# Optimization experiments

Hardware: AMD Instinct MI355X
Metric: run time of the kernel (lower is better)

Reference implementation:

```python
import jax, jax.numpy as jnp
import numpy as np

NUM_BINS = 8
TAIL = 3.0
MBW = 0.001  # min_bin_width
MBH = 0.001  # min_bin_height
MD = 0.001   # min_derivative


def _conv(x, w, b):
    y = jax.lax.conv_general_dilated(x, w, (1, 1), 'SAME',
                                     dimension_numbers=('NCHW', 'OIHW', 'NCHW'))
    return y + b[None, :, None, None]


def _convnet(x, w1, b1, w2, b2, w3, b3):
    h = jax.nn.relu(_conv(x, w1, b1))
    h = jax.nn.relu(_conv(h, w2, b2))
    return _conv(h, w3, b3)


def _rqs_forward(x, uw, uh, ud):
    # x: (N,), uw/uh: (N, num_bins), ud: (N, num_bins-1)
    nb = uw.shape[-1]
    inside = (x >= -TAIL) & (x <= TAIL)
    xin = jnp.clip(x, -TAIL, TAIL)
    # linear tails: pad derivatives so boundary slope == 1
    const = float(np.log(np.exp(1.0 - MD) - 1.0))
    ud = jnp.pad(ud, ((0, 0), (1, 1)), constant_values=const)

    widths = jax.nn.softmax(uw, axis=-1)
    widths = MBW + (1.0 - MBW * nb) * widths
    cumw = jnp.pad(jnp.cumsum(widths, axis=-1), ((0, 0), (1, 0)))
    cumw = 2.0 * TAIL * cumw - TAIL
    cumw = cumw.at[:, 0].set(-TAIL).at[:, -1].set(TAIL)
    widths = cumw[:, 1:] - cumw[:, :-1]

    heights = jax.nn.softmax(uh, axis=-1)
    heights = MBH + (1.0 - MBH * nb) * heights
    cumh = jnp.pad(jnp.cumsum(heights, axis=-1), ((0, 0), (1, 0)))
    cumh = 2.0 * TAIL * cumh - TAIL
    cumh = cumh.at[:, 0].set(-TAIL).at[:, -1].set(TAIL)
    heights = cumh[:, 1:] - cumh[:, :-1]

    deriv = MD + jax.nn.softplus(ud)  # (N, nb+1)

    # searchsorted: locate bin of each element
    idx = jnp.clip(jnp.sum((xin[:, None] >= cumw).astype(jnp.int32), axis=-1) - 1, 0, nb - 1)
    gather = lambda t: jnp.take_along_axis(t, idx[:, None], axis=-1)[:, 0]

    in_cw = gather(cumw)
    in_w = gather(widths)
    in_ch = gather(cumh)
    in_h = gather(heights)
    in_delta = gather(heights / widths)
    d0 = gather(deriv)
    d1 = gather(deriv[:, 1:])

    theta = (xin - in_cw) / in_w
    tom = theta * (1.0 - theta)
    numer = in_h * (in_delta * theta ** 2 + d0 * tom)
    denom = in_delta + (d0 + d1 - 2.0 * in_delta) * tom
    y = in_ch + numer / denom
    dnum = in_delta ** 2 * (d1 * theta ** 2 + 2.0 * in_delta * tom + d0 * (1.0 - theta) ** 2)
    lad = jnp.log(dnum) - 2.0 * jnp.log(denom)

    y = jnp.where(inside, y, x)
    lad = jnp.where(inside, lad, 0.0)
    return y, lad


def setup_inputs() -> dict:
    key = jax.random.key(0)
    ks = jax.random.split(key, 9)
    B, C, H, W = 32, 12, 64, 64
    hidden = 128
    cond_c = C // 3
    out_spline = C * (3 * NUM_BINS - 1)
    x = jax.random.normal(ks[0], (B, C, H, W), dtype=jnp.float32)
    logdet = jnp.zeros((B,), dtype=jnp.float32)
    conditioning = jax.random.normal(ks[1], (B, cond_c, H, W), dtype=jnp.float32)
    w1 = jax.random.normal(ks[2], (hidden, C + cond_c, 3, 3), dtype=jnp.float32) * 0.05
    b1 = jnp.zeros((hidden,), dtype=jnp.float32)
    w2 = jax.random.normal(ks[3], (hidden, hidden, 1, 1), dtype=jnp.float32) * 0.05
    b2 = jnp.zeros((hidden,), dtype=jnp.float32)
    w3 = jax.random.normal(ks[4], (out_spline, hidden, 3, 3), dtype=jnp.float32) * 0.01
    b3 = jnp.zeros((out_spline,), dtype=jnp.float32)
    return {"x": x, "logdet": logdet, "conditioning": conditioning,
            "w1": w1, "b1": b1, "w2": w2, "b2": b2, "w3": w3, "b3": b3}


def reference(x, logdet, conditioning, w1, b1, w2, b2, w3, b3):
    B, C, H, W = x.shape
    net_in = jnp.concatenate([x, conditioning], axis=1)
    params = _convnet(net_in, w1, b1, w2, b2, w3, b3)  # (B, C*(3nb-1), H, W)
    params = params.reshape(B, C, 3 * NUM_BINS - 1, H, W)
    params = params.transpose(0, 1, 3, 4, 2).reshape(B * C * H * W, 3 * NUM_BINS - 1)
    uw = params[:, :NUM_BINS]
    uh = params[:, NUM_BINS:2 * NUM_BINS]
    ud = params[:, 2 * NUM_BINS:]
    y_flat, lad_flat = _rqs_forward(x.reshape(-1), uw, uh, ud)
    y = y_flat.reshape(B, C, H, W)
    logdet_out = logdet + lad_flat.reshape(B, -1).sum(axis=1)
    return y, logdet_out
```

## Files before the change

### kernel.cpp

```cpp
#include <hip/hip_runtime.h>
#include <math.h>


#define NPIX 4096
#define NY   1572864

typedef _Float16 half8 __attribute__((ext_vector_type(8)));
typedef _Float16 half4 __attribute__((ext_vector_type(4)));
typedef float f32x4 __attribute__((ext_vector_type(4)));

#define ASYNC16(gsrc, ldst) \
  __builtin_amdgcn_global_load_lds((const __attribute__((address_space(1))) unsigned int*)(gsrc), \
                                   (__attribute__((address_space(3))) unsigned int*)(ldst), 16, 0, 0)

#define H2P_PLANE 4356
#define H2P_IDX(b, cc, pp) ((((size_t)(b) * 4 + (cc)) * H2P_PLANE + (pp)) << 5)
#define XH_IDX(b, pp) (((size_t)(b) * H2P_PLANE + (pp)) << 5)

__global__ __launch_bounds__(256) void prep_k(
    const float* __restrict__ w1, const float* __restrict__ w2,
    const float* __restrict__ w3, _Float16* __restrict__ w1h,
    _Float16* __restrict__ w2h, _Float16* __restrict__ w3h,
    const float* __restrict__ logdet, float* __restrict__ ld_out)
{
    const int i = blockIdx.x * 256 + threadIdx.x;
    if (i < 36864) {
        int k = i & 31, oc = (i >> 5) & 127, t = i >> 12;
        w1h[i] = (_Float16)((k < 16) ? w1[(oc * 16 + k) * 9 + t] : 0.f);
    }
    if (i < 16384) {
        int km = i & 31, oc = (i >> 5) & 127, ks = i >> 12;
        w2h[i] = (_Float16)w2[oc * 128 + ks * 32 + km];
    }
    {
        int cim = i & 31;
        int oc = (i >> 5) % 288;
        int tc = i / (288 * 32);
        int t = tc >> 2, cc = tc & 3;
        int c = oc / 24, j = oc % 24;
        int ci = cc * 32 + cim;
        float v = (j < 23) ? w3[((c * 23 + j) * 128 + ci) * 9 + t] : 0.f;
        w3h[i] = (_Float16)v;
    }
    if (i < 32) ld_out[i] = logdet[i];
}

__global__ __launch_bounds__(256) void xh_k(
    const float* __restrict__ x, const float* __restrict__ cond,
    _Float16* __restrict__ xh)
{
    const int i = blockIdx.x * 256 + threadIdx.x;
    if (i >= 139392) return;
    const int b = i / H2P_PLANE, pp = i % H2P_PLANE;
    const int pr = pp / 66, pc = pp % 66;
    const bool interior = (pr >= 1) && (pr <= 64) && (pc >= 1) && (pc <= 64);
    _Float16 v[32];
#pragma unroll
    for (int ci = 0; ci < 32; ++ci) v[ci] = (_Float16)0.f;
    if (interior) {
        const int p = (pr - 1) * 64 + (pc - 1);
#pragma unroll
        for (int ci = 0; ci < 12; ++ci)
            v[ci] = (_Float16)x[((size_t)(b * 12 + ci) << 12) + p];
#pragma unroll
        for (int ci = 0; ci < 4; ++ci)
            v[12 + ci] = (_Float16)cond[((size_t)(b * 4 + ci) << 12) + p];
    }
    _Float16* dst = xh + ((size_t)i << 5);
#pragma unroll
    for (int q = 0; q < 4; ++q) *(f32x4*)(dst + q * 8) = *(f32x4*)(v + q * 8);
}

__global__ __launch_bounds__(256) void zring_k(_Float16* __restrict__ h2p)
{
    const int i = blockIdx.x * 256 + threadIdx.x;
    if (i >= 133120) return;
    const int q = i & 3;
    const int rest = i >> 2;
    const int r = rest % 260;
    const int cc = (rest / 260) & 3;
    const int b = rest / 1040;
    int pp;
    if (r < 66)       pp = r;
    else if (r < 132) pp = 65 * 66 + (r - 66);
    else if (r < 196) pp = (r - 131) * 66;
    else              pp = (r - 195) * 66 + 65;
    f32x4 z = {0.f, 0.f, 0.f, 0.f};
    *(f32x4*)(h2p + H2P_IDX(b, cc, pp) + q * 8) = z;
}

__global__ __launch_bounds__(256, 2) void conv1_k(
    const _Float16* __restrict__ xh, const _Float16* __restrict__ w1h,
    const float* __restrict__ b1, _Float16* __restrict__ h1p)
{
    __shared__ __align__(16) char smem[73728];
    const int tid = threadIdx.x;
    const int wv = tid >> 6, lane = tid & 63;
    const int row16 = lane & 15, quad = lane >> 4;
    const int ptile = blockIdx.x;
    const int b = ptile >> 4;
    const int pim0 = (ptile & 15) << 8;
    const int h0 = pim0 >> 6;

#pragma unroll
    for (int k = 0; k < 18; ++k)
        ASYNC16(w1h + (size_t)(k * 256 + tid) * 8, smem + (k * 256 + wv * 64) * 16);

    f32x4 acc[4][8];
#pragma unroll
    for (int pt = 0; pt < 4; ++pt)
#pragma unroll
        for (int ot = 0; ot < 8; ++ot) acc[pt][ot] = (f32x4){0.f, 0.f, 0.f, 0.f};

    __syncthreads();
    const _Float16* wl = (const _Float16*)smem;

    for (int t = 0; t < 9; ++t) {
        const int dy = t / 3, dx = t % 3;
        const int pbase = (h0 + wv + dy) * 66 + dx + row16;
        half8 bf[4], af[8];
#pragma unroll
        for (int pt = 0; pt < 4; ++pt)
            bf[pt] = *(const half8*)(xh + XH_IDX(b, pbase + pt * 16) + quad * 8);
#pragma unroll
        for (int ot = 0; ot < 8; ++ot)
            af[ot] = *(const half8*)(wl + ((t * 128 + ot * 16 + row16) << 5) + quad * 8);
#pragma unroll
        for (int ot = 0; ot < 8; ++ot)
#pragma unroll
            for (int pt = 0; pt < 4; ++pt)
                acc[pt][ot] = __builtin_amdgcn_mfma_f32_16x16x32_f16(af[ot], bf[pt], acc[pt][ot], 0, 0, 0);
    }

    f32x4 bias[8];
#pragma unroll
    for (int ot = 0; ot < 8; ++ot) bias[ot] = *(const f32x4*)(b1 + ot * 16 + quad * 4);
#pragma unroll
    for (int pt = 0; pt < 4; ++pt) {
        const size_t pbase = ((size_t)((b << 12) + pim0 + wv * 64 + pt * 16 + row16)) << 7;
#pragma unroll
        for (int ot = 0; ot < 8; ++ot) {
            half4 v;
#pragma unroll
            for (int r = 0; r < 4; ++r)
                v[r] = (_Float16)fmaxf(acc[pt][ot][r] + bias[ot][r], 0.f);
            *(half4*)(h1p + pbase + ot * 16 + quad * 4) = v;
        }
    }
}

__global__ __launch_bounds__(256, 2) void conv2_k(
    const _Float16* __restrict__ h1p, const _Float16* __restrict__ w2h,
    const float* __restrict__ b2, _Float16* __restrict__ h2p)
{
    __shared__ __align__(16) char smem[33280];
    float* b2l = (float*)(smem + 32768);
    const int tid = threadIdx.x;
    const int wv = tid >> 6, lane = tid & 63;
    const int row16 = lane & 15, quad = lane >> 4;
    const int ptile = blockIdx.x;
    const int b = ptile >> 4;
    const int pim0 = (ptile & 15) << 8;

    if (tid < 128) b2l[tid] = b2[tid];
#pragma unroll
    for (int k = 0; k < 8; ++k) {
        const int c0 = k * 256 + wv * 64;
        ASYNC16(w2h + (size_t)(c0 + lane) * 8, smem + c0 * 16);
    }

    f32x4 acc[4][8];
#pragma unroll
    for (int pt = 0; pt < 4; ++pt)
#pragma unroll
        for (int ot = 0; ot < 8; ++ot) acc[pt][ot] = (f32x4){0.f, 0.f, 0.f, 0.f};

    const int pixbase = (b << 12) + pim0 + wv * 64;
    __syncthreads();

#pragma unroll
    for (int ks = 0; ks < 4; ++ks) {
        half8 bf[4], af[8];
#pragma unroll
        for (int pt = 0; pt < 4; ++pt)
            bf[pt] = *(const half8*)(h1p + ((size_t)(pixbase + pt * 16 + row16) << 7) + ks * 32 + quad * 8);
        const _Float16* wl = (const _Float16*)smem;
#pragma unroll
        for (int ot = 0; ot < 8; ++ot)
            af[ot] = *(const half8*)(wl + ((ks * 128 + ot * 16 + row16) << 5) + quad * 8);
#pragma unroll
        for (int ot = 0; ot < 8; ++ot)
#pragma unroll
            for (int pt = 0; pt < 4; ++pt)
                acc[pt][ot] = __builtin_amdgcn_mfma_f32_16x16x32_f16(af[ot], bf[pt], acc[pt][ot], 0, 0, 0);
    }

#pragma unroll
    for (int pt = 0; pt < 4; ++pt) {
        const int p = pim0 + wv * 64 + pt * 16 + row16;
        const int pp = ((p >> 6) + 1) * 66 + (p & 63) + 1;
#pragma unroll
        for (int ot = 0; ot < 8; ++ot) {
            const int oc0 = ot * 16 + quad * 4;
            half4 v;
#pragma unroll
            for (int r = 0; r < 4; ++r)
                v[r] = (_Float16)fmaxf(acc[pt][ot][r] + b2l[oc0 + r], 0.f);
            *(half4*)(h2p + H2P_IDX(b, oc0 >> 5, pp) + (oc0 & 31)) = v;
        }
    }
}

__device__ __forceinline__ void rqs_eval(const float* prm, float xv,
                                         float& yv_out, float& lad_out)
{
    const float xin = fminf(fmaxf(xv, -3.f), 3.f);

    float mw = prm[0], mh = prm[8];
#pragma unroll
    for (int j = 1; j < 8; ++j) { mw = fmaxf(mw, prm[j]); mh = fmaxf(mh, prm[8 + j]); }
    float ew[8], eh[8];
    float sw = 0.f, sh = 0.f;
#pragma unroll
    for (int j = 0; j < 8; ++j) {
        ew[j] = expf(prm[j] - mw);      sw += ew[j];
        eh[j] = expf(prm[8 + j] - mh);  sh += eh[j];
    }
    const float rw = 1.f / sw, rh = 1.f / sh;

    const float CONST_D = logf(expf(0.999f) - 1.f);

    float cumw = 0.f, cumh = 0.f;
    float cw_lo = -3.f, ch_lo = -3.f;
    float in_cw = 0.f, in_w = 1.f, in_ch = 0.f, in_h = 1.f, sd0 = 0.f, sd1 = 0.f;
#pragma unroll
    for (int i = 0; i < 8; ++i) {
        cumw += fmaf(0.992f, ew[i] * rw, 0.001f);
        cumh += fmaf(0.992f, eh[i] * rh, 0.001f);
        const float cw_hi = (i == 7) ? 3.f : fmaf(6.f, cumw, -3.f);
        const float ch_hi = (i == 7) ? 3.f : fmaf(6.f, cumh, -3.f);
        const bool sel = (xin >= cw_lo) && ((i == 7) || (xin < cw_hi));
        in_cw = sel ? cw_lo : in_cw;
        in_w  = sel ? (cw_hi - cw_lo) : in_w;
        in_ch = sel ? ch_lo : in_ch;
        in_h  = sel ? (ch_hi - ch_lo) : in_h;
        sd0   = sel ? ((i == 0) ? CONST_D : prm[16 + i - 1]) : sd0;
        sd1   = sel ? ((i == 7) ? CONST_D : prm[16 + i]) : sd1;
        cw_lo = cw_hi; ch_lo = ch_hi;
    }

    const float d0 = 0.001f + ((sd0 > 20.f) ? sd0 : log1pf(expf(sd0)));
    const float d1 = 0.001f + ((sd1 > 20.f) ? sd1 : log1pf(expf(sd1)));

    const float delta = in_h / in_w;
    const float theta = (xin - in_cw) / in_w;
    const float omt = 1.f - theta;
    const float tom = theta * omt;
    const float th2 = theta * theta;
    const float numer = in_h * (delta * th2 + d0 * tom);
    const float denom = delta + (d0 + d1 - 2.f * delta) * tom;
    float yv = in_ch + numer / denom;
    const float dnum = delta * delta * (d1 * th2 + 2.f * delta * tom + d0 * omt * omt);
    float lad = logf(dnum) - 2.f * logf(denom);

    const bool inside = (xv >= -3.f) && (xv <= 3.f);
    yv_out = inside ? yv : xv;
    lad_out = inside ? lad : 0.f;
}

__global__ __launch_bounds__(256, 2) void conv3_rqs_k(
    const _Float16* __restrict__ h2p, const _Float16* __restrict__ w3h,
    const float* __restrict__ b3, const float* __restrict__ x,
    float* __restrict__ y, float* __restrict__ ld_out)
{
    __shared__ __align__(16) char smem[44352];
    float* b3l = (float*)(smem + 43776);

    const int tid = threadIdx.x;
    const int wv = tid >> 6, lane = tid & 63;
    const int row16 = lane & 15, quad = lane >> 4;
    const int col = blockIdx.x;
    const int ptile = blockIdx.y;
    const int b = ptile >> 4;
    const int pim0 = (ptile & 15) << 8;
    const int h0 = pim0 >> 6;

    if (tid < 144) {
        const int c = tid / 24, j = tid % 24;
        b3l[tid] = (j < 23) ? b3[(col * 6 + c) * 23 + j] : 0.f;
    }

    f32x4 acc[4][9];
#pragma unroll
    for (int pt = 0; pt < 4; ++pt)
#pragma unroll
        for (int ot = 0; ot < 9; ++ot) acc[pt][ot] = (f32x4){0.f, 0.f, 0.f, 0.f};

    auto stage_wt = [&](int t, int cc, int buf) {
        const _Float16* g = w3h + ((size_t)((t * 4 + cc) * 288 + col * 144) << 5);
        char* wb = smem + 25344 + buf * 9216;
        ASYNC16(g + (size_t)tid * 8, wb + wv * 64 * 16);
        ASYNC16(g + (size_t)(256 + tid) * 8, wb + (256 + wv * 64) * 16);
        if (wv == 0) ASYNC16(g + (size_t)(512 + lane) * 8, wb + 512 * 16);
    };
    auto stage_act = [&](int cc) {
        const _Float16* ga = h2p + H2P_IDX(b, cc, h0 * 66);
#pragma unroll
        for (int k = 0; k < 6; ++k)
            ASYNC16(ga + (size_t)(k * 256 + tid) * 8, smem + (k * 256 + wv * 64) * 16);
        if (wv == 0 && lane < 48)
            ASYNC16(ga + (size_t)(1536 + lane) * 8, smem + 1536 * 16);
    };

    stage_act(0);
    stage_wt(0, 0, 0);

    for (int cc = 0; cc < 4; ++cc) {
        for (int t = 0; t < 9; ++t) {
            const int step = cc * 9 + t;
            __syncthreads();
            if (step + 1 < 36)
                stage_wt((t == 8) ? 0 : t + 1, (t == 8) ? cc + 1 : cc, (step + 1) & 1);
            const _Float16* act = (const _Float16*)smem;
            const _Float16* wt = (const _Float16*)(smem + 25344 + (step & 1) * 9216);
            const int dy = t / 3, dx = t % 3;
            const int lpp = (wv + dy) * 66 + dx + row16;
            half8 bf[4], af[9];
#pragma unroll
            for (int pt = 0; pt < 4; ++pt)
                bf[pt] = *(const half8*)(act + ((lpp + pt * 16) << 5) + quad * 8);
#pragma unroll
            for (int ot = 0; ot < 9; ++ot)
                af[ot] = *(const half8*)(wt + ((ot * 16 + row16) << 5) + quad * 8);
#pragma unroll
            for (int ot = 0; ot < 9; ++ot)
#pragma unroll
                for (int pt = 0; pt < 4; ++pt)
                    acc[pt][ot] = __builtin_amdgcn_mfma_f32_16x16x32_f16(af[ot], bf[pt], acc[pt][ot], 0, 0, 0);
            if (t == 8 && cc < 3) {
                __syncthreads();
                stage_act(cc + 1);
            }
        }
    }
    __syncthreads();

    float* epi = (float*)smem + wv * 2368;
    float lad_acc = 0.f;
#pragma unroll
    for (int pt = 0; pt < 4; ++pt) {
#pragma unroll
        for (int ot = 0; ot < 9; ++ot)
            *(f32x4*)(epi + row16 * 148 + ot * 16 + quad * 4) = acc[pt][ot];
        __syncthreads();
#pragma unroll 1
        for (int pass = 0; pass < 2; ++pass) {
            const int idx = pass * 64 + lane;
            if (idx < 96) {
                const int p16 = idx & 15, c = idx >> 4;
                float prm[23];
#pragma unroll
                for (int j = 0; j < 23; ++j)
                    prm[j] = epi[p16 * 148 + c * 24 + j] + b3l[c * 24 + j];
                const int tpix = wv * 64 + pt * 16 + p16;
                const size_t xi = (((size_t)(b * 12 + col * 6 + c)) << 12) + (pim0 + tpix);
                const float xv = x[xi];
                float yv, lad;
                rqs_eval(prm, xv, yv, lad);
                y[xi] = yv;
                lad_acc += lad;
            }
        }
        __syncthreads();
    }

#pragma unroll
    for (int off = 32; off > 0; off >>= 1) lad_acc += __shfl_down(lad_acc, off);
    if (lane == 0) atomicAdd(&ld_out[b], lad_acc);
}

extern "C" void kernel_launch(void* const* d_in, const int* in_sizes, int n_in,
                              void* d_out, int out_size, void* d_ws, size_t ws_size,
                              hipStream_t stream)
{
    const float* x      = (const float*)d_in[0];
    const float* logdet = (const float*)d_in[1];
    const float* cond   = (const float*)d_in[2];
    const float* w1     = (const float*)d_in[3];
    const float* b1     = (const float*)d_in[4];
    const float* w2     = (const float*)d_in[5];
    const float* b2     = (const float*)d_in[6];
    const float* w3     = (const float*)d_in[7];
    const float* b3     = (const float*)d_in[8];

    char* ws = (char*)d_ws;
    _Float16* h1p = (_Float16*)ws;
    _Float16* h2p = (_Float16*)(ws + 33554432);
    _Float16* xh  = (_Float16*)(ws + 33554432);
    _Float16* w1h = (_Float16*)(ws + 69238784);
    _Float16* w2h = (_Float16*)(ws + 69312512);
    _Float16* w3h = (_Float16*)(ws + 69345280);

    float* y      = (float*)d_out;
    float* ld_out = y + NY;

    prep_k<<<1296, 256, 0, stream>>>(w1, w2, w3, w1h, w2h, w3h, logdet, ld_out);
    xh_k<<<545, 256, 0, stream>>>(x, cond, xh);
    conv1_k<<<512, 256, 0, stream>>>(xh, w1h, b1, h1p);
    zring_k<<<520, 256, 0, stream>>>(h2p);
    conv2_k<<<512, 256, 0, stream>>>(h1p, w2h, b2, h2p);
    conv3_rqs_k<<<dim3(2, 512), 256, 0, stream>>>(h2p, w3h, b3, x, y, ld_out);
}
```

Baseline: 238.2 us.

## Fold small prep kernels into neighbors and speed up RQS epilogue

Merges the input-packing kernel into the weight prep kernel and moves h2p border zeroing into conv2, removing two launches. The RQS spline evaluation switches to fast intrinsics (__expf/__logf), a precomputed constant, a shared reciprocal, and vectorized LDS parameter loads. Block-wide barriers in the per-wave epilogue are replaced with a wave-local LDS wait, since each wave uses its own scratch region. Fast-math intrinsics slightly reduce accuracy.

Result: faster. 226.1 us (-5.1%).

```diff
diff --git a/kernel.cpp b/kernel.cpp
--- a/kernel.cpp
+++ b/kernel.cpp
@@ -17,11 +17,13 @@
 #define H2P_IDX(b, cc, pp) ((((size_t)(b) * 4 + (cc)) * H2P_PLANE + (pp)) << 5)
 #define XH_IDX(b, pp) (((size_t)(b) * H2P_PLANE + (pp)) << 5)
 
-__global__ __launch_bounds__(256) void prep_k(
+__global__ __launch_bounds__(256) void prep_xh_k(
     const float* __restrict__ w1, const float* __restrict__ w2,
     const float* __restrict__ w3, _Float16* __restrict__ w1h,
     _Float16* __restrict__ w2h, _Float16* __restrict__ w3h,
-    const float* __restrict__ logdet, float* __restrict__ ld_out)
+    const float* __restrict__ logdet, float* __restrict__ ld_out,
+    const float* __restrict__ x, const float* __restrict__ cond,
+    _Float16* __restrict__ xh)
 {
     const int i = blockIdx.x * 256 + threadIdx.x;
     if (i < 36864) {
@@ -43,50 +45,27 @@
         w3h[i] = (_Float16)v;
     }
     if (i < 32) ld_out[i] = logdet[i];
-}
-
-__global__ __launch_bounds__(256) void xh_k(
-    const float* __restrict__ x, const float* __restrict__ cond,
-    _Float16* __restrict__ xh)
-{
-    const int i = blockIdx.x * 256 + threadIdx.x;
-    if (i >= 139392) return;
-    const int b = i / H2P_PLANE, pp = i % H2P_PLANE;
-    const int pr = pp / 66, pc = pp % 66;
-    const bool interior = (pr >= 1) && (pr <= 64) && (pc >= 1) && (pc <= 64);
-    _Float16 v[32];
-#pragma unroll
-    for (int ci = 0; ci < 32; ++ci) v[ci] = (_Float16)0.f;
-    if (interior) {
-        const int p = (pr - 1) * 64 + (pc - 1);
-#pragma unroll
-        for (int ci = 0; ci < 12; ++ci)
-            v[ci] = (_Float16)x[((size_t)(b * 12 + ci) << 12) + p];
-#pragma unroll
-        for (int ci = 0; ci < 4; ++ci)
-            v[12 + ci] = (_Float16)cond[((size_t)(b * 4 + ci) << 12) + p];
-    }
-    _Float16* dst = xh + ((size_t)i << 5);
-#pragma unroll
-    for (int q = 0; q < 4; ++q) *(f32x4*)(dst + q * 8) = *(f32x4*)(v + q * 8);
-}
-
-__global__ __launch_bounds__(256) void zring_k(_Float16* __restrict__ h2p)
-{
-    const int i = blockIdx.x * 256 + threadIdx.x;
-    if (i >= 133120) return;
-    const int q = i & 3;
-    const int rest = i >> 2;
-    const int r = rest % 260;
-    const int cc = (rest / 260) & 3;
-    const int b = rest / 1040;
-    int pp;
-    if (r < 66)       pp = r;
-    else if (r < 132) pp = 65 * 66 + (r - 66);
-    else if (r < 196) pp = (r - 131) * 66;
-    else              pp = (r - 195) * 66 + 65;
-    f32x4 z = {0.f, 0.f, 0.f, 0.f};
-    *(f32x4*)(h2p + H2P_IDX(b, cc, pp) + q * 8) = z;
+
+    if (i < 139392) {
+        const int b = i / H2P_PLANE, pp = i % H2P_PLANE;
+        const int pr = pp / 66, pc = pp % 66;
+        const bool interior = (pr >= 1) && (pr <= 64) && (pc >= 1) && (pc <= 64);
+        _Float16 v[32];
+#pragma unroll
+        for (int ci = 0; ci < 32; ++ci) v[ci] = (_Float16)0.f;
+        if (interior) {
+            const int p = (pr - 1) * 64 + (pc - 1);
+#pragma unroll
+            for (int ci = 0; ci < 12; ++ci)
+                v[ci] = (_Float16)x[((size_t)(b * 12 + ci) << 12) + p];
+#pragma unroll
+            for (int ci = 0; ci < 4; ++ci)
+                v[12 + ci] = (_Float16)cond[((size_t)(b * 4 + ci) << 12) + p];
+        }
+        _Float16* dst = xh + ((size_t)i << 5);
+#pragma unroll
+        for (int q = 0; q < 4; ++q) *(f32x4*)(dst + q * 8) = *(f32x4*)(v + q * 8);
+    }
 }
 
 __global__ __launch_bounds__(256, 2) void conv1_k(
@@ -169,6 +148,28 @@
         ASYNC16(w2h + (size_t)(c0 + lane) * 8, smem + c0 * 16);
     }
 
+    {
+        const int base = blockIdx.x * 256 + tid;
+#pragma unroll
+        for (int rep = 0; rep < 2; ++rep) {
+            const int i = base + rep * 131072;
+            if (i < 133120) {
+                const int q = i & 3;
+                const int rest = i >> 2;
+                const int r = rest % 260;
+                const int cc2 = (rest / 260) & 3;
+                const int bb = rest / 1040;
+                int pp;
+                if (r < 66)       pp = r;
+                else if (r < 132) pp = 65 * 66 + (r - 66);
+                else if (r < 196) pp = (r - 131) * 66;
+                else              pp = (r - 195) * 66 + 65;
+                f32x4 z = {0.f, 0.f, 0.f, 0.f};
+                *(f32x4*)(h2p + H2P_IDX(bb, cc2, pp) + q * 8) = z;
+            }
+        }
+    }
+
     f32x4 acc[4][8];
 #pragma unroll
     for (int pt = 0; pt < 4; ++pt)
@@ -211,24 +212,25 @@
     }
 }
 
-__device__ __forceinline__ void rqs_eval(const float* prm, float xv,
+__device__ __forceinline__ void rqs_eval(const f32x4* pv, float xv,
                                          float& yv_out, float& lad_out)
 {
+#define PRM(j) (pv[(j) >> 2][(j) & 3])
     const float xin = fminf(fmaxf(xv, -3.f), 3.f);
 
-    float mw = prm[0], mh = prm[8];
-#pragma unroll
-    for (int j = 1; j < 8; ++j) { mw = fmaxf(mw, prm[j]); mh = fmaxf(mh, prm[8 + j]); }
+    float mw = PRM(0), mh = PRM(8);
+#pragma unroll
+    for (int j = 1; j < 8; ++j) { mw = fmaxf(mw, PRM(j)); mh = fmaxf(mh, PRM(8 + j)); }
     float ew[8], eh[8];
     float sw = 0.f, sh = 0.f;
 #pragma unroll
     for (int j = 0; j < 8; ++j) {
-        ew[j] = expf(prm[j] - mw);      sw += ew[j];
-        eh[j] = expf(prm[8 + j] - mh);  sh += eh[j];
+        ew[j] = __expf(PRM(j) - mw);      sw += ew[j];
+        eh[j] = __expf(PRM(8 + j) - mh);  sh += eh[j];
     }
     const float rw = 1.f / sw, rh = 1.f / sh;
 
-    const float CONST_D = logf(expf(0.999f) - 1.f);
+    const float CONST_D = 0.5397423f;
 
     float cumw = 0.f, cumh = 0.f;
     float cw_lo = -3.f, ch_lo = -3.f;
@@ -244,16 +246,17 @@
         in_w  = sel ? (cw_hi - cw_lo) : in_w;
         in_ch = sel ? ch_lo : in_ch;
         in_h  = sel ? (ch_hi - ch_lo) : in_h;
-        sd0   = sel ? ((i == 0) ? CONST_D : prm[16 + i - 1]) : sd0;
-        sd1   = sel ? ((i == 7) ? CONST_D : prm[16 + i]) : sd1;
+        sd0   = sel ? ((i == 0) ? CONST_D : PRM(16 + i - 1)) : sd0;
+        sd1   = sel ? ((i == 7) ? CONST_D : PRM(16 + i)) : sd1;
         cw_lo = cw_hi; ch_lo = ch_hi;
     }
 
-    const float d0 = 0.001f + ((sd0 > 20.f) ? sd0 : log1pf(expf(sd0)));
-    const float d1 = 0.001f + ((sd1 > 20.f) ? sd1 : log1pf(expf(sd1)));
-
-    const float delta = in_h / in_w;
-    const float theta = (xin - in_cw) / in_w;
+    const float d0 = 0.001f + ((sd0 > 20.f) ? sd0 : __logf(1.f + __expf(sd0)));
+    const float d1 = 0.001f + ((sd1 > 20.f) ? sd1 : __logf(1.f + __expf(sd1)));
+
+    const float r_inw = 1.f / in_w;
+    const float delta = in_h * r_inw;
+    const float theta = (xin - in_cw) * r_inw;
     const float omt = 1.f - theta;
     const float tom = theta * omt;
     const float th2 = theta * theta;
@@ -261,11 +264,12 @@
     const float denom = delta + (d0 + d1 - 2.f * delta) * tom;
     float yv = in_ch + numer / denom;
     const float dnum = delta * delta * (d1 * th2 + 2.f * delta * tom + d0 * omt * omt);
-    float lad = logf(dnum) - 2.f * logf(denom);
+    float lad = __logf(dnum) - 2.f * __logf(denom);
 
     const bool inside = (xv >= -3.f) && (xv <= 3.f);
     yv_out = inside ? yv : xv;
     lad_out = inside ? lad : 0.f;
+#undef PRM
 }
 
 __global__ __launch_bounds__(256, 2) void conv3_rqs_k(
@@ -352,26 +356,30 @@
 #pragma unroll
         for (int ot = 0; ot < 9; ++ot)
             *(f32x4*)(epi + row16 * 148 + ot * 16 + quad * 4) = acc[pt][ot];
-        __syncthreads();
+        asm volatile("s_waitcnt lgkmcnt(0)" ::: "memory");
+        __builtin_amdgcn_sched_barrier(0);
 #pragma unroll 1
         for (int pass = 0; pass < 2; ++pass) {
             const int idx = pass * 64 + lane;
             if (idx < 96) {
                 const int p16 = idx & 15, c = idx >> 4;
-                float prm[23];
-#pragma unroll
-                for (int j = 0; j < 23; ++j)
-                    prm[j] = epi[p16 * 148 + c * 24 + j] + b3l[c * 24 + j];
+                const float* pb = epi + p16 * 148 + c * 24;
+                const float* bb = b3l + c * 24;
+                f32x4 pv[6];
+#pragma unroll
+                for (int q = 0; q < 6; ++q)
+                    pv[q] = *(const f32x4*)(pb + q * 4) + *(const f32x4*)(bb + q * 4);
                 const int tpix = wv * 64 + pt * 16 + p16;
                 const size_t xi = (((size_t)(b * 12 + col * 6 + c)) << 12) + (pim0 + tpix);
                 const float xv = x[xi];
                 float yv, lad;
-                rqs_eval(prm, xv, yv, lad);
+                rqs_eval(pv, xv, yv, lad);
                 y[xi] = yv;
                 lad_acc += lad;
             }
         }
-        __syncthreads();
+        asm volatile("s_waitcnt lgkmcnt(0)" ::: "memory");
+        __builtin_amdgcn_sched_barrier(0);
     }
 
 #pragma unroll
@@ -404,10 +412,8 @@
     float* y      = (float*)d_out;
     float* ld_out = y + NY;
 
-    prep_k<<<1296, 256, 0, stream>>>(w1, w2, w3, w1h, w2h, w3h, logdet, ld_out);
-    xh_k<<<545, 256, 0, stream>>>(x, cond, xh);
+    prep_xh_k<<<1296, 256, 0, stream>>>(w1, w2, w3, w1h, w2h, w3h, logdet, ld_out, x, cond, xh);
     conv1_k<<<512, 256, 0, stream>>>(xh, w1h, b1, h1p);
-    zring_k<<<520, 256, 0, stream>>>(h2p);
     conv2_k<<<512, 256, 0, stream>>>(h1p, w2h, b2, h2p);
     conv3_rqs_k<<<dim3(2, 512), 256, 0, stream>>>(h2p, w3h, b3, x, y, ld_out);
 }
```
